# Performance work log

Measured on AMD Instinct MI355X. Metric: run time of the kernel, lower is better.

The kernel has to match this reference:

```python
import jax, jax.numpy as jnp
import numpy as np

N_HEAD = 16

def setup_inputs() -> dict:
    key = jax.random.key(0)
    k1, k2, k3, k4, k5 = jax.random.split(key, 5)
    B, T, C = 2, 2048, 1024
    x = jax.random.normal(k1, (B, T, C), dtype=jnp.float32)
    s = 0.02
    W_attn = jax.random.normal(k2, (C, 3 * C), dtype=jnp.float32) * s
    b_attn = jnp.zeros((3 * C,), dtype=jnp.float32)
    W_proj = jax.random.normal(k3, (C, C), dtype=jnp.float32) * s
    b_proj = jnp.zeros((C,), dtype=jnp.float32)
    return {"x": x, "W_attn": W_attn, "b_attn": b_attn, "W_proj": W_proj, "b_proj": b_proj}

def reference(x, W_attn, b_attn, W_proj, b_proj):
    B, T, C = x.shape
    H = N_HEAD
    hd = C // H
    qkv = x @ W_attn + b_attn                      # (B,T,3C)
    q, k, v = jnp.split(qkv, 3, axis=-1)
    # (B,T,C) -> (B,H,T,hd)
    def to_heads(t):
        return t.reshape(B, T, H, hd).transpose(0, 2, 1, 3)
    q, k, v = to_heads(q), to_heads(k), to_heads(v)
    scale = 1.0 / jnp.sqrt(jnp.asarray(hd, dtype=x.dtype))
    att = jnp.einsum('bhqd,bhkd->bhqk', q, k) * scale  # (B,H,T,T)
    causal = jnp.tril(jnp.ones((T, T), dtype=bool))
    att = jnp.where(causal[None, None], att, -jnp.inf)
    att = jax.nn.softmax(att, axis=-1)
    y = jnp.einsum('bhqk,bhkd->bhqd', att, v)          # (B,H,T,hd)
    y = y.transpose(0, 2, 1, 3).reshape(B, T, C)
    return y @ W_proj + b_proj
```

## Files before the change

kernel.cpp:

```cpp
#include <hip/hip_runtime.h>

#define N_HEAD 16

typedef __attribute__((ext_vector_type(8))) __bf16 bf16x8;
typedef __attribute__((ext_vector_type(8))) short  s16x8;
typedef __attribute__((ext_vector_type(4))) short  s16x4;
typedef __attribute__((ext_vector_type(4))) float  f32x4;
typedef __attribute__((ext_vector_type(4))) unsigned u32x4;

#if __has_builtin(__builtin_amdgcn_exp2f)
#define EXP2(x) __builtin_amdgcn_exp2f(x)
#else
#define EXP2(x) exp2f(x)
#endif
#if __has_builtin(__builtin_amdgcn_rcpf)
#define RCP(x) __builtin_amdgcn_rcpf(x)
#else
#define RCP(x) (1.0f / (x))
#endif

static __device__ __forceinline__ short f2bf(float f) {
    unsigned u = __builtin_bit_cast(unsigned, f);
    unsigned r = (u + 0x7FFFu + ((u >> 16) & 1u)) >> 16;
    return (short)r;
}

static __device__ __forceinline__ unsigned cvt_pk_bf16(float lo, float hi) {
    unsigned d;
    asm("v_cvt_pk_bf16_f32 %0, %1, %2" : "=v"(d) : "v"(lo), "v"(hi));
    return d;
}

static __device__ __forceinline__ void gload_lds16(const void* g, void* l) {
    __builtin_amdgcn_global_load_lds(
        (const __attribute__((address_space(1))) void*)g,
        (__attribute__((address_space(3))) void*)l, 16, 0, 0);
}

#define BARX() do { asm volatile("" ::: "memory"); __builtin_amdgcn_s_barrier(); \
                    asm volatile("" ::: "memory"); } while (0)
#define VMCNT4() asm volatile("s_waitcnt vmcnt(4)" ::: "memory")
#define VMCNT0() asm volatile("s_waitcnt vmcnt(0)" ::: "memory")

__global__ __launch_bounds__(256) void cvt_bf16(
    const float* __restrict__ X, short* __restrict__ Y, int n)
{
    int idx = blockIdx.x * 256 + threadIdx.x;
    size_t base = (size_t)idx * 8;
    if (base + 8 > (size_t)n) return;
    float4 f0 = *(const float4*)&X[base];
    float4 f1 = *(const float4*)&X[base + 4];
    s16x8 o;
    o[0] = f2bf(f0.x); o[1] = f2bf(f0.y); o[2] = f2bf(f0.z); o[3] = f2bf(f0.w);
    o[4] = f2bf(f1.x); o[5] = f2bf(f1.y); o[6] = f2bf(f1.z); o[7] = f2bf(f1.w);
    *(s16x8*)&Y[base] = o;
}

__global__ __launch_bounds__(256) void transpose_w(
    const float* __restrict__ W, short* __restrict__ Wt, int N, int K)
{
    __shared__ short Ts[64][72];
    const int n0 = blockIdx.x * 64, k0 = blockIdx.y * 64;
    const int tid = threadIdx.x;
    const int r = tid >> 4, c4 = (tid & 15) * 4;
#pragma unroll
    for (int i = 0; i < 4; ++i) {
        int row = r + i * 16;
        float4 f = *(const float4*)&W[(size_t)(k0 + row) * N + n0 + c4];
        s16x4 s = { f2bf(f.x), f2bf(f.y), f2bf(f.z), f2bf(f.w) };
        *(s16x4*)&Ts[row][c4] = s;
    }
    __syncthreads();
#pragma unroll
    for (int i = 0; i < 4; ++i) {
        int row = r + i * 16;
        s16x4 s = { Ts[c4 + 0][row], Ts[c4 + 1][row], Ts[c4 + 2][row], Ts[c4 + 3][row] };
        *(s16x4*)&Wt[(size_t)(n0 + row) * K + k0 + c4] = s;
    }
}

__global__ __launch_bounds__(256) void qkv_gemm(
    const short* __restrict__ Xb,
    const short* __restrict__ Wt,
    const float* __restrict__ bias,
    short* __restrict__ Qo, short* __restrict__ Ko, short* __restrict__ Vo)
{
    __shared__ short As[3 * 4096];
    __shared__ short Bs[3 * 4096];
    const int tid = threadIdx.x, wave = tid >> 6, lane = tid & 63;
    const int row0 = blockIdx.x * 128, col0 = blockIdx.y * 128;
    const int srow = wave * 16 + (lane >> 2);
    const int sc = (((lane & 3) ^ ((lane >> 3) & 3)) * 8);
    const short* aS = Xb + (size_t)(row0 + srow) * 1024 + sc;
    const short* bS = Wt + (size_t)(col0 + srow) * 1024 + sc;
    const int woff = wave * 512;
    const int wr = (wave >> 1) * 64, wc = (wave & 1) * 64;
    const int arow = lane & 15, g = lane >> 4;
    const int foff = (g ^ ((arow >> 1) & 3)) * 8;

    f32x4 acc[4][4] = {};

#define STAGE(T, BUF) do { const size_t _k = (size_t)(T) * 32; \
    gload_lds16(aS + _k,             As + (BUF) * 4096 + woff); \
    gload_lds16(aS + _k + 64 * 1024, As + (BUF) * 4096 + woff + 2048); \
    gload_lds16(bS + _k,             Bs + (BUF) * 4096 + woff); \
    gload_lds16(bS + _k + 64 * 1024, Bs + (BUF) * 4096 + woff + 2048); \
} while (0)

#define COMPUTE(BUF) do { \
    bf16x8 af[4], bfr[4]; \
    _Pragma("unroll") \
    for (int i = 0; i < 4; ++i) af[i]  = *(const bf16x8*)&As[(BUF) * 4096 + (wr + i * 16 + arow) * 32 + foff]; \
    _Pragma("unroll") \
    for (int j = 0; j < 4; ++j) bfr[j] = *(const bf16x8*)&Bs[(BUF) * 4096 + (wc + j * 16 + arow) * 32 + foff]; \
    _Pragma("unroll") \
    for (int i = 0; i < 4; ++i) \
        _Pragma("unroll") \
        for (int j = 0; j < 4; ++j) \
            acc[i][j] = __builtin_amdgcn_mfma_f32_16x16x32_bf16(af[i], bfr[j], acc[i][j], 0, 0, 0); \
} while (0)

    STAGE(0, 0); STAGE(1, 1);
    VMCNT4(); BARX();

    int cur = 0;
    for (int t = 0; t < 30; ++t) {
        int nbuf = cur + 2; if (nbuf >= 3) nbuf -= 3;
        STAGE(t + 2, nbuf);
        COMPUTE(cur);
        VMCNT4(); BARX();
        cur = (cur == 2) ? 0 : cur + 1;
    }
    COMPUTE(cur); VMCNT0(); BARX();
    cur = (cur == 2) ? 0 : cur + 1;
    COMPUTE(cur);
#undef STAGE
#undef COMPUTE

    const int which = col0 >> 10;
    const int bb = row0 >> 11;
    const int ccol = arow, crow = g * 4;
#pragma unroll
    for (int j = 0; j < 4; ++j) {
        int n = col0 + wc + j * 16 + ccol;
        float bv = bias[n];
        int nc = n & 1023, head = nc >> 6, hd = nc & 63;
        if (which == 0) {
#pragma unroll
            for (int i = 0; i < 4; ++i) {
                int t0 = (row0 & 2047) + wr + i * 16 + crow;
#pragma unroll
                for (int r = 0; r < 4; ++r)
                    Qo[((size_t)(bb * N_HEAD + head) * 2048 + t0 + r) * 64 + hd] =
                        f2bf((acc[i][j][r] + bv) * 0.18033688f);
            }
        } else if (which == 1) {
#pragma unroll
            for (int i = 0; i < 4; ++i) {
                int t0 = (row0 & 2047) + wr + i * 16 + crow;
#pragma unroll
                for (int r = 0; r < 4; ++r)
                    Ko[((size_t)(bb * N_HEAD + head) * 2048 + t0 + r) * 64 + hd] =
                        f2bf(acc[i][j][r] + bv);
            }
        } else {
#pragma unroll
            for (int i = 0; i < 4; ++i) {
                int t0 = (row0 & 2047) + wr + i * 16 + crow;
                s16x4 ov = { f2bf(acc[i][j][0] + bv), f2bf(acc[i][j][1] + bv),
                             f2bf(acc[i][j][2] + bv), f2bf(acc[i][j][3] + bv) };
                *(s16x4*)&Vo[((size_t)(bb * N_HEAD + head) * 64 + hd) * 2048 + t0] = ov;
            }
        }
    }
}

__global__ __launch_bounds__(256) void attn_kernel(
    const short* __restrict__ Q, const short* __restrict__ K,
    const short* __restrict__ Vt, short* __restrict__ Y)
{
    __shared__ short Ks[2][64 * 64];
    __shared__ short Vs[2][64 * 64];
    const int bh = blockIdx.x;
    const int qt = gridDim.y - 1 - blockIdx.y;
    const int q0 = qt * 64;
    const int b = bh >> 4, h = bh & 15;
    const short* Qh = Q  + (size_t)bh * 2048 * 64;
    const short* Kh = K  + (size_t)bh * 2048 * 64;
    const short* Vh = Vt + (size_t)bh * 64 * 2048;
    const int tid = threadIdx.x, wave = tid >> 6, lane = tid & 63;
    const int qrow0 = q0 + wave * 16;
    const int arow = lane & 15, g = lane >> 4;

    const int rho = wave * 16 + (lane >> 3);
    const int kappa = ((rho >> 5) << 5) | (((rho >> 2) & 3) << 3)
                    | (((rho >> 4) & 1) << 2) | (rho & 3);
    const int xchunk = 8 * ((lane & 7) ^ (rho & 7));
    const short* kSrc = Kh + (size_t)kappa * 64 + xchunk;
    const short* vSrc = Vh + (size_t)rho * 2048 + xchunk;

    bf16x8 qfr[2];
#pragma unroll
    for (int c = 0; c < 2; ++c)
        qfr[c] = *(const bf16x8*)&Qh[(size_t)(qrow0 + arow) * 64 + c * 32 + (g * 8)];

    f32x4 o[4] = {};
    float lsum = 0.f;

    const int nt = qt + 1;

    gload_lds16(kSrc,            Ks[0] + wave * 1024);
    gload_lds16(kSrc + 1024,     Ks[0] + wave * 1024 + 512);
    gload_lds16(vSrc,            Vs[0] + wave * 1024);
    gload_lds16(vSrc + 8 * 2048, Vs[0] + wave * 1024 + 512);
    __syncthreads();

    int cur = 0;
    for (int t = 0; t < nt; ++t) {
        const int kt = t << 6;
        if (t + 1 < nt) {
            const int kn = kt + 64;
            short* kD = Ks[cur ^ 1] + wave * 1024;
            short* vD = Vs[cur ^ 1] + wave * 1024;
            gload_lds16(kSrc + (size_t)kn * 64,        kD);
            gload_lds16(kSrc + (size_t)kn * 64 + 1024, kD + 512);
            gload_lds16(vSrc + kn,                     vD);
            gload_lds16(vSrc + kn + 8 * 2048,          vD + 512);
        }
        if (kt <= qrow0 + 15) {
            const short* Kc = Ks[cur];
            const short* Vc = Vs[cur];
            const bool need_mask = (kt + 64) > qrow0;
            f32x4 s[4] = {};
#pragma unroll
            for (int kc = 0; kc < 4; ++kc) {
                int krow = kc * 16 + arow;
                int xr = krow & 7;
#pragma unroll
                for (int c = 0; c < 2; ++c) {
                    bf16x8 kf = *(const bf16x8*)&Kc[krow * 64 + (((c * 4 + g) ^ xr) * 8)];
                    s[kc] = __builtin_amdgcn_mfma_f32_16x16x32_bf16(kf, qfr[c], s[kc], 0, 0, 0);
                }
            }
            if (need_mask) {
                int q = qrow0 + arow;
#pragma unroll
                for (int kc = 0; kc < 4; ++kc) {
                    int keyb = kt + ((kc >> 1) << 5) + (g << 3) + ((kc & 1) << 2);
#pragma unroll
                    for (int r = 0; r < 4; ++r)
                        if (keyb + r > q) s[kc][r] = -3.0e38f;
                }
            }
            unsigned pa[8];
#pragma unroll
            for (int kc = 0; kc < 4; ++kc) {
                float p0 = EXP2(s[kc][0]);
                float p1 = EXP2(s[kc][1]);
                float p2 = EXP2(s[kc][2]);
                float p3 = EXP2(s[kc][3]);
                lsum += (p0 + p1) + (p2 + p3);
                pa[kc * 2 + 0] = cvt_pk_bf16(p0, p1);
                pa[kc * 2 + 1] = cvt_pk_bf16(p2, p3);
            }
#pragma unroll
            for (int c = 0; c < 2; ++c) {
                bf16x8 pb = __builtin_bit_cast(bf16x8,
                    (u32x4){ pa[4 * c], pa[4 * c + 1], pa[4 * c + 2], pa[4 * c + 3] });
#pragma unroll
                for (int j = 0; j < 4; ++j) {
                    int d = j * 16 + arow;
                    bf16x8 vf = *(const bf16x8*)&Vc[d * 64 + (((c * 4 + g) ^ (d & 7)) * 8)];
                    o[j] = __builtin_amdgcn_mfma_f32_16x16x32_bf16(vf, pb, o[j], 0, 0, 0);
                }
            }
        }
        __syncthreads();
        cur ^= 1;
    }

    {
        float l = lsum;
        l += __shfl_xor(l, 16);
        l += __shfl_xor(l, 32);
        float li = RCP(l);
        int t = qrow0 + arow;
#pragma unroll
        for (int j = 0; j < 4; ++j) {
            s16x4 ov = { f2bf(o[j][0] * li), f2bf(o[j][1] * li),
                         f2bf(o[j][2] * li), f2bf(o[j][3] * li) };
            *(s16x4*)&Y[((size_t)(b * 2048 + t)) * 1024 + h * 64 + j * 16 + 4 * g] = ov;
        }
    }
}

__global__ __launch_bounds__(256) void proj_gemm(
    const short* __restrict__ Yb,
    const short* __restrict__ Wpt,
    const float* __restrict__ bias,
    float* __restrict__ Out)
{
    __shared__ short As[3 * 4096];
    __shared__ short Bs[3 * 4096];
    const int tid = threadIdx.x, wave = tid >> 6, lane = tid & 63;
    const int row0 = blockIdx.x * 128, col0 = blockIdx.y * 128;
    const int srow = wave * 16 + (lane >> 2);
    const int sc = (((lane & 3) ^ ((lane >> 3) & 3)) * 8);
    const short* aS = Yb  + (size_t)(row0 + srow) * 1024 + sc;
    const short* bS = Wpt + (size_t)(col0 + srow) * 1024 + sc;
    const int woff = wave * 512;
    const int wr = (wave >> 1) * 64, wc = (wave & 1) * 64;
    const int arow = lane & 15, g = lane >> 4;
    const int foff = (g ^ ((arow >> 1) & 3)) * 8;

    f32x4 acc[4][4] = {};

#define STAGE(T, BUF) do { const size_t _k = (size_t)(T) * 32; \
    gload_lds16(aS + _k,             As + (BUF) * 4096 + woff); \
    gload_lds16(aS + _k + 64 * 1024, As + (BUF) * 4096 + woff + 2048); \
    gload_lds16(bS + _k,             Bs + (BUF) * 4096 + woff); \
    gload_lds16(bS + _k + 64 * 1024, Bs + (BUF) * 4096 + woff + 2048); \
} while (0)

#define COMPUTE(BUF) do { \
    bf16x8 af[4], bfr[4]; \
    _Pragma("unroll") \
    for (int i = 0; i < 4; ++i) af[i]  = *(const bf16x8*)&As[(BUF) * 4096 + (wr + i * 16 + arow) * 32 + foff]; \
    _Pragma("unroll") \
    for (int j = 0; j < 4; ++j) bfr[j] = *(const bf16x8*)&Bs[(BUF) * 4096 + (wc + j * 16 + arow) * 32 + foff]; \
    _Pragma("unroll") \
    for (int i = 0; i < 4; ++i) \
        _Pragma("unroll") \
        for (int j = 0; j < 4; ++j) \
            acc[i][j] = __builtin_amdgcn_mfma_f32_16x16x32_bf16(af[i], bfr[j], acc[i][j], 0, 0, 0); \
} while (0)

    STAGE(0, 0); STAGE(1, 1);
    VMCNT4(); BARX();

    int cur = 0;
    for (int t = 0; t < 30; ++t) {
        int nbuf = cur + 2; if (nbuf >= 3) nbuf -= 3;
        STAGE(t + 2, nbuf);
        COMPUTE(cur);
        VMCNT4(); BARX();
        cur = (cur == 2) ? 0 : cur + 1;
    }
    COMPUTE(cur); VMCNT0(); BARX();
    cur = (cur == 2) ? 0 : cur + 1;
    COMPUTE(cur);
#undef STAGE
#undef COMPUTE

    const int ccol = arow, crow = g * 4;
#pragma unroll
    for (int i = 0; i < 4; ++i)
#pragma unroll
        for (int j = 0; j < 4; ++j)
#pragma unroll
            for (int r = 0; r < 4; ++r) {
                int m = row0 + wr + i * 16 + crow + r;
                int n = col0 + wc + j * 16 + ccol;
                Out[(size_t)m * 1024 + n] = acc[i][j][r] + bias[n];
            }
}

extern "C" void kernel_launch(void* const* d_in, const int* in_sizes, int n_in,
                              void* d_out, int out_size, void* d_ws, size_t ws_size,
                              hipStream_t stream) {
    const float* x      = (const float*)d_in[0];
    const float* W_attn = (const float*)d_in[1];
    const float* b_attn = (const float*)d_in[2];
    const float* W_proj = (const float*)d_in[3];
    const float* b_proj = (const float*)d_in[4];
    float* out = (float*)d_out;

    short* Xb  = (short*)d_ws;
    short* Wat = Xb + 4194304;
    short* Wpt = Wat + 3145728;
    short* qb  = Wpt + 1048576;
    short* kb  = qb + 4194304;
    short* vb  = kb + 4194304;
    short* yb  = Xb;

    cvt_bf16<<<2048, 256, 0, stream>>>(x, Xb, 4194304);
    transpose_w<<<dim3(48, 16), 256, 0, stream>>>(W_attn, Wat, 3072, 1024);
    transpose_w<<<dim3(16, 16), 256, 0, stream>>>(W_proj, Wpt, 1024, 1024);
    qkv_gemm<<<dim3(32, 24), 256, 0, stream>>>(Xb, Wat, b_attn, qb, kb, vb);
    attn_kernel<<<dim3(32, 32), 256, 0, stream>>>(qb, kb, vb, yb);
    proj_gemm<<<dim3(32, 8), 256, 0, stream>>>(yb, Wpt, b_proj, out);
}
```

Measured before the change: 118.2 us.

## Merge prep kernels, reorder attention q-tiles, simplify proj_gemm to double buffering

Folds the fp32-to-bf16 conversion of x and both weight transposes into one prep launch to save launch overhead. Replaces the reversed query-tile order in the attention kernel with an interleaved permutation so long and short causal tiles are mixed across the schedule, aiming for better load balance. Rewrites the proj_gemm main loop from a three-stage pipeline with explicit vmcnt waits to a simpler two-buffer loop with __syncthreads each step. That loop may lose some latency hiding, and __syncthreads may not wait for the global_load_lds transfers the way the explicit vmcnt did.

```diff
diff --git a/kernel.cpp b/kernel.cpp
--- a/kernel.cpp
+++ b/kernel.cpp
@@ -42,26 +42,26 @@
 #define VMCNT4() asm volatile("s_waitcnt vmcnt(4)" ::: "memory")
 #define VMCNT0() asm volatile("s_waitcnt vmcnt(0)" ::: "memory")
 
-__global__ __launch_bounds__(256) void cvt_bf16(
-    const float* __restrict__ X, short* __restrict__ Y, int n)
-{
-    int idx = blockIdx.x * 256 + threadIdx.x;
-    size_t base = (size_t)idx * 8;
-    if (base + 8 > (size_t)n) return;
-    float4 f0 = *(const float4*)&X[base];
-    float4 f1 = *(const float4*)&X[base + 4];
-    s16x8 o;
-    o[0] = f2bf(f0.x); o[1] = f2bf(f0.y); o[2] = f2bf(f0.z); o[3] = f2bf(f0.w);
-    o[4] = f2bf(f1.x); o[5] = f2bf(f1.y); o[6] = f2bf(f1.z); o[7] = f2bf(f1.w);
-    *(s16x8*)&Y[base] = o;
-}
-
-__global__ __launch_bounds__(256) void transpose_w(
-    const float* __restrict__ W, short* __restrict__ Wt, int N, int K)
+__global__ __launch_bounds__(256) void prep(
+    const float* __restrict__ X,  short* __restrict__ Xb,
+    const float* __restrict__ Wa, short* __restrict__ Wat,
+    const float* __restrict__ Wp, short* __restrict__ Wpt)
 {
     __shared__ short Ts[64][72];
-    const int n0 = blockIdx.x * 64, k0 = blockIdx.y * 64;
-    const int tid = threadIdx.x;
+    const int bid = blockIdx.x, tid = threadIdx.x;
+    if (bid < 2048) {
+        size_t base = ((size_t)bid * 256 + tid) * 8;
+        float4 f0 = *(const float4*)&X[base];
+        float4 f1 = *(const float4*)&X[base + 4];
+        s16x8 o;
+        o[0] = f2bf(f0.x); o[1] = f2bf(f0.y); o[2] = f2bf(f0.z); o[3] = f2bf(f0.w);
+        o[4] = f2bf(f1.x); o[5] = f2bf(f1.y); o[6] = f2bf(f1.z); o[7] = f2bf(f1.w);
+        *(s16x8*)&Xb[base] = o;
+        return;
+    }
+    const float* W; short* Wt; int N, n0, k0;
+    if (bid < 2816) { int rr = bid - 2048; W = Wa; Wt = Wat; N = 3072; n0 = (rr % 48) * 64; k0 = (rr / 48) * 64; }
+    else            { int rr = bid - 2816; W = Wp; Wt = Wpt; N = 1024; n0 = (rr % 16) * 64; k0 = (rr / 16) * 64; }
     const int r = tid >> 4, c4 = (tid & 15) * 4;
 #pragma unroll
     for (int i = 0; i < 4; ++i) {
@@ -75,7 +75,7 @@
     for (int i = 0; i < 4; ++i) {
         int row = r + i * 16;
         s16x4 s = { Ts[c4 + 0][row], Ts[c4 + 1][row], Ts[c4 + 2][row], Ts[c4 + 3][row] };
-        *(s16x4*)&Wt[(size_t)(n0 + row) * K + k0 + c4] = s;
+        *(s16x4*)&Wt[(size_t)(n0 + row) * 1024 + k0 + c4] = s;
     }
 }
 
@@ -182,7 +182,8 @@
     __shared__ short Ks[2][64 * 64];
     __shared__ short Vs[2][64 * 64];
     const int bh = blockIdx.x;
-    const int qt = gridDim.y - 1 - blockIdx.y;
+    const int by = blockIdx.y, ba = by >> 3, bq = by & 7;
+    const int qt = (ba == 0) ? bq : (ba == 1) ? (31 - bq) : (ba == 2) ? (8 + bq) : (23 - bq);
     const int q0 = qt * 64;
     const int b = bh >> 4, h = bh & 15;
     const short* Qh = Q  + (size_t)bh * 2048 * 64;
@@ -300,8 +301,8 @@
     const float* __restrict__ bias,
     float* __restrict__ Out)
 {
-    __shared__ short As[3 * 4096];
-    __shared__ short Bs[3 * 4096];
+    __shared__ short As[2][4096];
+    __shared__ short Bs[2][4096];
     const int tid = threadIdx.x, wave = tid >> 6, lane = tid & 63;
     const int row0 = blockIdx.x * 128, col0 = blockIdx.y * 128;
     const int srow = wave * 16 + (lane >> 2);
@@ -315,42 +316,33 @@
 
     f32x4 acc[4][4] = {};
 
-#define STAGE(T, BUF) do { const size_t _k = (size_t)(T) * 32; \
-    gload_lds16(aS + _k,             As + (BUF) * 4096 + woff); \
-    gload_lds16(aS + _k + 64 * 1024, As + (BUF) * 4096 + woff + 2048); \
-    gload_lds16(bS + _k,             Bs + (BUF) * 4096 + woff); \
-    gload_lds16(bS + _k + 64 * 1024, Bs + (BUF) * 4096 + woff + 2048); \
-} while (0)
-
-#define COMPUTE(BUF) do { \
-    bf16x8 af[4], bfr[4]; \
-    _Pragma("unroll") \
-    for (int i = 0; i < 4; ++i) af[i]  = *(const bf16x8*)&As[(BUF) * 4096 + (wr + i * 16 + arow) * 32 + foff]; \
-    _Pragma("unroll") \
-    for (int j = 0; j < 4; ++j) bfr[j] = *(const bf16x8*)&Bs[(BUF) * 4096 + (wc + j * 16 + arow) * 32 + foff]; \
-    _Pragma("unroll") \
-    for (int i = 0; i < 4; ++i) \
-        _Pragma("unroll") \
-        for (int j = 0; j < 4; ++j) \
-            acc[i][j] = __builtin_amdgcn_mfma_f32_16x16x32_bf16(af[i], bfr[j], acc[i][j], 0, 0, 0); \
-} while (0)
-
-    STAGE(0, 0); STAGE(1, 1);
-    VMCNT4(); BARX();
+    gload_lds16(aS,             As[0] + woff);
+    gload_lds16(aS + 64 * 1024, As[0] + woff + 2048);
+    gload_lds16(bS,             Bs[0] + woff);
+    gload_lds16(bS + 64 * 1024, Bs[0] + woff + 2048);
+    __syncthreads();
 
     int cur = 0;
-    for (int t = 0; t < 30; ++t) {
-        int nbuf = cur + 2; if (nbuf >= 3) nbuf -= 3;
-        STAGE(t + 2, nbuf);
-        COMPUTE(cur);
-        VMCNT4(); BARX();
-        cur = (cur == 2) ? 0 : cur + 1;
-    }
-    COMPUTE(cur); VMCNT0(); BARX();
-    cur = (cur == 2) ? 0 : cur + 1;
-    COMPUTE(cur);
-#undef STAGE
-#undef COMPUTE
+    for (int k0 = 0; k0 < 1024; k0 += 32) {
+        if (k0 + 32 < 1024) {
+            gload_lds16(aS + k0 + 32,             As[cur ^ 1] + woff);
+            gload_lds16(aS + k0 + 32 + 64 * 1024, As[cur ^ 1] + woff + 2048);
+            gload_lds16(bS + k0 + 32,             Bs[cur ^ 1] + woff);
+            gload_lds16(bS + k0 + 32 + 64 * 1024, Bs[cur ^ 1] + woff + 2048);
+        }
+        bf16x8 af[4], bfr[4];
+#pragma unroll
+        for (int i = 0; i < 4; ++i) af[i]  = *(const bf16x8*)&As[cur][(wr + i * 16 + arow) * 32 + foff];
+#pragma unroll
+        for (int j = 0; j < 4; ++j) bfr[j] = *(const bf16x8*)&Bs[cur][(wc + j * 16 + arow) * 32 + foff];
+#pragma unroll
+        for (int i = 0; i < 4; ++i)
+#pragma unroll
+            for (int j = 0; j < 4; ++j)
+                acc[i][j] = __builtin_amdgcn_mfma_f32_16x16x32_bf16(af[i], bfr[j], acc[i][j], 0, 0, 0);
+        __syncthreads();
+        cur ^= 1;
+    }
 
     const int ccol = arow, crow = g * 4;
 #pragma unroll
@@ -383,9 +375,7 @@
     short* vb  = kb + 4194304;
     short* yb  = Xb;
 
-    cvt_bf16<<<2048, 256, 0, stream>>>(x, Xb, 4194304);
-    transpose_w<<<dim3(48, 16), 256, 0, stream>>>(W_attn, Wat, 3072, 1024);
-    transpose_w<<<dim3(16, 16), 256, 0, stream>>>(W_proj, Wpt, 1024, 1024);
+    prep<<<3072, 256, 0, stream>>>(x, Xb, W_attn, Wat, W_proj, Wpt);
     qkv_gemm<<<dim3(32, 24), 256, 0, stream>>>(Xb, Wat, b_attn, qb, kb, vb);
     attn_kernel<<<dim3(32, 32), 256, 0, stream>>>(qb, kb, vb, yb);
     proj_gemm<<<dim3(32, 8), 256, 0, stream>>>(yb, Wpt, b_proj, out);
```

Measured after the change: 104.3 us. -11.8%, faster.
